# Kernel tuning notes

Hardware: AMD Instinct MI355X
Metric: run time of the kernel (lower is better)

## Reference

```python
import jax, jax.numpy as jnp
import numpy as np

B, S, D, H = 2, 2048, 1024, 16
HD = D // H

def setup_inputs() -> dict:
    key = jax.random.key(0)
    ks = jax.random.split(key, 9)
    s = 1.0 / np.sqrt(D)
    inp = {"x": jax.random.normal(ks[0], (B, S, D), dtype=jnp.float32)}
    for i, name in enumerate(["q", "k", "v", "o"]):
        inp[f"W_{name}"] = jax.random.uniform(ks[1 + 2 * i], (D, D), dtype=jnp.float32, minval=-s, maxval=s)
        inp[f"b_{name}"] = jax.random.uniform(ks[2 + 2 * i], (D,), dtype=jnp.float32, minval=-s, maxval=s)
    return inp


def reference(x, W_q, b_q, W_k, b_k, W_v, b_v, W_o, b_o):
    # x: [B, S, D]
    def split_heads(t):
        return t.reshape(B, S, H, HD).transpose(0, 2, 1, 3)  # [B, H, S, HD]

    Q = split_heads(x @ W_q + b_q)
    K = split_heads(x @ W_k + b_k)
    V = split_heads(x @ W_v + b_v)

    scale = 1.0 / np.sqrt(HD).astype(np.float32)
    scores = jnp.einsum("bhqd,bhkd->bhqk", Q, K) * scale  # [B, H, S, S]
    weights = jax.nn.softmax(scores, axis=-1)
    attn = jnp.einsum("bhqk,bhkd->bhqd", weights, V)  # [B, H, S, HD]
    attn = attn.transpose(0, 2, 1, 3).reshape(B, S, D)
    return attn @ W_o + b_o
```

## Files before the change

### kernel.cpp

```cpp
#include <hip/hip_runtime.h>
#include <hip/hip_bf16.h>

#define BB 2
#define SS 2048
#define DD 1024
#define HH 16
#define HD 64

typedef __attribute__((ext_vector_type(8))) short bf16x8;
typedef __attribute__((ext_vector_type(4))) float f32x4;

__device__ __forceinline__ unsigned short f2bf(float f) {
  unsigned int u = __float_as_uint(f);
  return (unsigned short)((u + 0x7FFFu + ((u >> 16) & 1u)) >> 16);
}

__device__ __forceinline__ float fast_exp2(float x) {
#if __has_builtin(__builtin_amdgcn_exp2f)
  return __builtin_amdgcn_exp2f(x);
#else
  return __expf(x * 0.6931471805599453f);
#endif
}

__device__ __forceinline__ void async_copy16(const unsigned short* gp, unsigned short* lp) {
  __builtin_amdgcn_global_load_lds(
      (const __attribute__((address_space(1))) unsigned int*)gp,
      (__attribute__((address_space(3))) unsigned int*)lp, 16, 0, 0);
}

__device__ __forceinline__ void pl32_swap(unsigned& a, unsigned& b) {
#if __has_builtin(__builtin_amdgcn_permlane32_swap)
  auto r = __builtin_amdgcn_permlane32_swap(a, b, false, false);
  a = r[0];
  b = r[1];
#else
  asm volatile("v_permlane32_swap_b32 %0, %1" : "+v"(a), "+v"(b));
#endif
}
__device__ __forceinline__ void pl16_swap(unsigned& a, unsigned& b) {
#if __has_builtin(__builtin_amdgcn_permlane16_swap)
  auto r = __builtin_amdgcn_permlane16_swap(a, b, false, false);
  a = r[0];
  b = r[1];
#else
  asm volatile("v_permlane16_swap_b32 %0, %1" : "+v"(a), "+v"(b));
#endif
}

__global__ __launch_bounds__(256) void prep_kernel(
    const float* __restrict__ x, unsigned short* __restrict__ xb,
    const float* __restrict__ W0, unsigned short* __restrict__ T0,
    const float* __restrict__ W1, unsigned short* __restrict__ T1,
    const float* __restrict__ W2, unsigned short* __restrict__ T2,
    const float* __restrict__ W3, unsigned short* __restrict__ T3) {
  const int blk = blockIdx.x;
  const int t = threadIdx.x;
  if (blk < 4096) {
    int i = blk * 1024 + t * 4;
    float4 v = *(const float4*)(x + i);
    ushort4 u;
    u.x = f2bf(v.x); u.y = f2bf(v.y); u.z = f2bf(v.z); u.w = f2bf(v.w);
    *(ushort4*)(xb + i) = u;
    return;
  }
  const int j = blk - 4096;
  const int jw = j >> 10;
  const int tb = j & 1023;
  const float* W = jw == 0 ? W0 : (jw == 1 ? W1 : (jw == 2 ? W2 : W3));
  unsigned short* T = jw == 0 ? T0 : (jw == 1 ? T1 : (jw == 2 ? T2 : T3));
  __shared__ float tile[32][33];
  int k0 = (tb & 31) * 32, n0 = (tb >> 5) * 32;
  int c = t & 31, r0 = t >> 5;
#pragma unroll
  for (int i = 0; i < 4; ++i) {
    int r = r0 + i * 8;
    tile[r][c] = W[(size_t)(k0 + r) * DD + n0 + c];
  }
  __syncthreads();
#pragma unroll
  for (int i = 0; i < 4; ++i) {
    int r = r0 + i * 8;
    T[(size_t)(n0 + r) * DD + k0 + c] = f2bf(tile[c][r]);
  }
}

template <int STORE>
__device__ __forceinline__ void gemm_core(
    const unsigned short* __restrict__ A, const unsigned short* __restrict__ BT,
    const float* __restrict__ bias, void* __restrict__ outp, float scale,
    int bm, int bn) {
  const int t = threadIdx.x;
  const int w = t >> 6;
  const int l = t & 63;
  const int wm = (w >> 1) * 64;
  const int wn = (w & 1) * 64;

  __shared__ __align__(16) unsigned short As[128 * 32];
  __shared__ __align__(16) unsigned short Bs[128 * 32];

  f32x4 acc[4][4];
#pragma unroll
  for (int i = 0; i < 4; ++i)
#pragma unroll
    for (int j = 0; j < 4; ++j) acc[i][j] = (f32x4)0.f;

  const int fr = l & 15;
  const int kg = (l >> 4) * 8;

  for (int k0 = 0; k0 < DD; k0 += 32) {
    __syncthreads();
#pragma unroll
    for (int c = 0; c < 2; ++c) {
      int e = (w * 2 + c) * 512 + l * 8;
      int row = e >> 5, kk = e & 31;
      async_copy16(A + (size_t)(bm + row) * DD + k0 + kk, As + (w * 2 + c) * 512);
      async_copy16(BT + (size_t)(bn + row) * DD + k0 + kk, Bs + (w * 2 + c) * 512);
    }
    __syncthreads();

    bf16x8 af[4], bfr[4];
#pragma unroll
    for (int i = 0; i < 4; ++i)
      af[i] = *(const bf16x8*)(As + (wm + i * 16 + fr) * 32 + kg);
#pragma unroll
    for (int j = 0; j < 4; ++j)
      bfr[j] = *(const bf16x8*)(Bs + (wn + j * 16 + fr) * 32 + kg);
#pragma unroll
    for (int i = 0; i < 4; ++i)
#pragma unroll
      for (int j = 0; j < 4; ++j)
        acc[i][j] = __builtin_amdgcn_mfma_f32_16x16x32_bf16(af[i], bfr[j], acc[i][j], 0, 0, 0);
  }

  const int col_l = l & 15;
  const int row_l = (l >> 4) * 4;

#pragma unroll
  for (int i = 0; i < 4; ++i) {
    int m_base = bm + wm + i * 16 + row_l;
#pragma unroll
    for (int j = 0; j < 4; ++j) {
      int n = bn + wn + j * 16 + col_l;
      float bv = bias[n];
      float* out = (float*)outp;
#pragma unroll
      for (int r = 0; r < 4; ++r)
        out[(size_t)(m_base + r) * DD + n] = acc[i][j][r] + bv;
    }
  }
}

__global__ __launch_bounds__(256) void out_gemm_mfma(
    const unsigned short* __restrict__ A, const unsigned short* __restrict__ WoT,
    const float* __restrict__ bo, float* __restrict__ out) {
  const int i = blockIdx.x;
  const int xcd = i & 7;
  const int slot = i >> 3;
  const int bm = (xcd + 8 * (slot >> 3)) * 128;
  const int bn = (slot & 7) * 128;
  gemm_core<0>(A, WoT, bo, (void*)out, 1.0f, bm, bn);
}

#define QPHASE(DB, KH, MH, S, VM) do {                                        \
    bf16x8 af[4];                                                             \
    _Pragma("unroll")                                                         \
    for (int ii = 0; ii < 4; ++ii) {                                          \
      int row = wm * 128 + (MH) * 64 + ii * 16 + fr;                          \
      int kb = kg16 ^ ((row & 8) ? 32 : 0) ^ ((row & 4) ? 16 : 0);            \
      af[ii] = *(const bf16x8*)((const char*)&lds[0][DB][KH][0] + row * 64 + kb); \
    }                                                                         \
    if ((MH) == 0) {                                                          \
      _Pragma("unroll")                                                       \
      for (int j = 0; j < 4; ++j) {                                           \
        int row = wn * 64 + j * 16 + fr;                                      \
        int kb = kg16 ^ ((row & 8) ? 32 : 0) ^ ((row & 4) ? 16 : 0);          \
        bfr[j] = *(const bf16x8*)((const char*)&lds[1][DB][KH][0] + row * 64 + kb); \
      }                                                                       \
    }                                                                         \
    stage_half(S);                                                            \
    asm volatile("s_barrier" ::: "memory");                                   \
    __builtin_amdgcn_s_setprio(1);                                            \
    _Pragma("unroll")                                                         \
    for (int ii = 0; ii < 4; ++ii)                                            \
      _Pragma("unroll")                                                       \
      for (int j = 0; j < 4; ++j)                                             \
        acc[(MH) * 4 + ii][j] = __builtin_amdgcn_mfma_f32_16x16x32_bf16(      \
            af[ii], bfr[j], acc[(MH) * 4 + ii][j], 0, 0, 0);                  \
    __builtin_amdgcn_s_setprio(0);                                            \
    if ((VM) == 1) asm volatile("s_waitcnt vmcnt(4)" ::: "memory");           \
    if ((VM) == 2) asm volatile("s_waitcnt vmcnt(0)" ::: "memory");           \
    asm volatile("s_barrier" ::: "memory");                                   \
  } while (0)

__global__ __launch_bounds__(512, 2) void qkv_gemm_8ph(
    const unsigned short* __restrict__ A,
    const unsigned short* __restrict__ WqT, const unsigned short* __restrict__ WkT,
    const unsigned short* __restrict__ WvT,
    const float* __restrict__ bq, const float* __restrict__ bk,
    const float* __restrict__ bv,
    unsigned short* __restrict__ Qo, unsigned short* __restrict__ Ko,
    unsigned short* __restrict__ VTo) {
  const int i = blockIdx.x;
  const int xcd = i & 7;
  const int slot = i >> 3;
  const int bmi = xcd * 2 + (slot / 12);
  const int c = slot % 12;
  const int which = c >> 2;
  const int bm = bmi * 256;
  const int bn = (c & 3) * 256;
  const unsigned short* BT = which == 0 ? WqT : (which == 1 ? WkT : WvT);
  const float* bias = which == 0 ? bq : (which == 1 ? bk : bv);

  const int t = threadIdx.x;
  const int w = t >> 6;
  const int l = t & 63;
  const int wm = w >> 2;
  const int wn = w & 3;
  const int fr = l & 15;
  const int kg16 = (l >> 4) * 16;

  __shared__ __align__(16) unsigned short lds[2][2][2][8192];

  f32x4 acc[8][4];
#pragma unroll
  for (int mi = 0; mi < 8; ++mi)
#pragma unroll
    for (int j = 0; j < 4; ++j) acc[mi][j] = (f32x4)0.f;

  auto stage_half = [&](int s) {
    if (s >= 64) return;
    const int Ts = s >> 2;
    const int db = Ts & 1;
    const int typ = s & 3;
    const int kh = typ >> 1;
    const int isB = typ & 1;
    const unsigned short* src = isB ? BT : A;
    const int rbase = isB ? bn : bm;
    unsigned short* dstbase = &lds[isB][db][kh][0];
    const int k0 = Ts * 64 + kh * 32;
#pragma unroll
    for (int j = 0; j < 2; ++j) {
      int cc = (w * 2 + j) * 64 + l;
      int row = cc >> 2;
      int ke = ((cc & 3) * 8) ^ ((row & 8) ? 16 : 0) ^ ((row & 4) ? 8 : 0);
      async_copy16(src + (size_t)(rbase + row) * DD + k0 + ke,
                   dstbase + (w * 2 + j) * 512);
    }
  };

  bf16x8 bfr[4];

  for (int s = 0; s < 6; ++s) stage_half(s);
  asm volatile("s_waitcnt vmcnt(4)" ::: "memory");
  asm volatile("s_barrier" ::: "memory");

  for (int T = 0; T < 14; ++T) {
    const int db = T & 1;
    const int sb = 4 * T + 6;
    QPHASE(db, 0, 0, sb + 0, 0);
    QPHASE(db, 0, 1, sb + 1, 0);
    QPHASE(db, 1, 0, sb + 2, 0);
    QPHASE(db, 1, 1, sb + 3, 1);
  }
  QPHASE(0, 0, 0, 62, 0);
  QPHASE(0, 0, 1, 63, 0);
  QPHASE(0, 1, 0, 64, 0);
  QPHASE(0, 1, 1, 64, 2);
  QPHASE(1, 0, 0, 64, 0);
  QPHASE(1, 0, 1, 64, 0);
  QPHASE(1, 1, 0, 64, 0);
  QPHASE(1, 1, 1, 64, 0);

  const int col_l = l & 15;
  const int row_l = (l >> 4) * 4;
  const int b_ = bm >> 11;

  if (which != 2) {
    const float scl = which == 0 ? 0.18033688011112042f : 1.0f;
    unsigned short* out = which == 0 ? Qo : Ko;
#pragma unroll
    for (int mi = 0; mi < 8; ++mi) {
      int m_base = bm + wm * 128 + mi * 16 + row_l;
#pragma unroll
      for (int j = 0; j < 4; ++j) {
        int n = bn + wn * 64 + j * 16 + col_l;
        float bv = bias[n];
        int h_ = n >> 6, hd_ = n & 63;
#pragma unroll
        for (int r = 0; r < 4; ++r) {
          int m = m_base + r;
          int b2 = m >> 11, s_ = m & 2047;
          out[(((size_t)(b2 * HH + h_) * SS) + s_) * HD + hd_] =
              f2bf((acc[mi][j][r] + bv) * scl);
        }
      }
    }
  } else {
    unsigned int* Tt = (unsigned int*)&lds[0][0][0][0];
#pragma unroll
    for (int mi = 0; mi < 8; ++mi) {
      int m2a = wm * 64 + mi * 8 + (l >> 4) * 2;
#pragma unroll
      for (int j = 0; j < 4; ++j) {
        int n = wn * 64 + j * 16 + col_l;
        float bv = bias[bn + n];
        uint2 dd;
        dd.x = (unsigned)f2bf(acc[mi][j][0] + bv) |
               ((unsigned)f2bf(acc[mi][j][1] + bv) << 16);
        dd.y = (unsigned)f2bf(acc[mi][j][2] + bv) |
               ((unsigned)f2bf(acc[mi][j][3] + bv) << 16);
        *(uint2*)(Tt + n * 128 + (m2a ^ ((n & 7) << 2))) = dd;
      }
    }
    __syncthreads();
    const int srow0 = bm & 2047;
    const int n_r = t >> 1;
    const int half = t & 1;
    const int n_glob = bn + n_r;
    const int h_ = n_glob >> 6, hd_ = n_glob & 63;
    unsigned short* ob =
        VTo + ((size_t)((b_ * HH + h_) * HD + hd_)) * SS + srow0 + half * 128;
#pragma unroll
    for (int cp = 0; cp < 16; ++cp) {
      uint4 v = *(const uint4*)(Tt + n_r * 128 +
                                ((half * 64 + cp * 4) ^ ((n_r & 7) << 2)));
      *(uint4*)(ob + cp * 8) = v;
    }
  }
}

__global__ __launch_bounds__(512, 4) void flash_attn_mfma(
    const unsigned short* __restrict__ Q,
    const unsigned short* __restrict__ K,
    const unsigned short* __restrict__ VT,
    unsigned short* __restrict__ ctx) {
  const int bh = blockIdx.x;
  const int qt = blockIdx.y;
  const int b  = bh >> 4;
  const int h  = bh & 15;
  const int t  = threadIdx.x;
  const int w  = t >> 6;
  const int l  = t & 63;
  const int wg = w & 3;
  const int wh = w >> 2;
  const int g  = l >> 4;
  const int ln = l & 15;

  const unsigned short* Qp = Q + ((size_t)bh * SS + (size_t)qt * 64 + wg * 16) * HD;
  const unsigned short* Kp = K + (size_t)bh * SS * HD;
  const unsigned short* Vp = VT + (size_t)bh * HD * SS;

  __shared__ __align__(16) unsigned short smem[2][2][2][2048];
  __shared__ __align__(16) float rred[4 * 64];

  bf16x8 qf[2];
#pragma unroll
  for (int kb = 0; kb < 2; ++kb)
    qf[kb] = *(const bf16x8*)(Qp + ln * HD + kb * 32 + g * 8);

  f32x4 o[4];
#pragma unroll
  for (int mt = 0; mt < 4; ++mt) o[mt] = (f32x4)0.f;
  float rs = 0.f;

  const int sp  = w >> 2;
  const int sq  = w & 3;
  const int idx = sq * 64 + l;
  const int rowK = idx >> 3;
  const int gccK = (idx & 7) ^ (rowK & 7);
  const unsigned short* kgp = Kp + (size_t)(sp * 32 + rowK) * HD + gccK * 8;
  const int rowV = idx >> 2;
  const int gc2V = (idx & 3) ^ ((rowV >> 1) & 3);
  const unsigned short* vgp = Vp + (size_t)rowV * SS + sp * 32 + gc2V * 8;
  unsigned short* dK = &smem[0][sp][0][sq * 512];
  unsigned short* dV = &smem[1][sp][0][sq * 512];

  int ko[2][2];
#pragma unroll
  for (int kb = 0; kb < 2; ++kb)
#pragma unroll
    for (int mt = 0; mt < 2; ++mt) {
      int row = mt * 16 + ln;
      ko[kb][mt] = row * 128 + (((kb * 4 + g) ^ (row & 7)) * 16);
    }
  int vo[4];
#pragma unroll
  for (int mt = 0; mt < 4; ++mt) {
    int row = mt * 16 + ln;
    vo[mt] = row * 64 + ((g ^ ((row >> 1) & 3)) * 16);
  }
  const char* kpar = (const char*)&smem[0][wh][0][0];
  const char* vpar = (const char*)&smem[1][wh][0][0];

  auto stage_i = [&](int db) {
    async_copy16(kgp, dK + db * 2048);
    async_copy16(vgp, dV + db * 2048);
    kgp += 64 * HD;
    vgp += 64;
  };

  auto body = [&](int db) {
    const char* Kst = kpar + db * 4096;
    const char* Vst = vpar + db * 4096;

    f32x4 st[2];
#pragma unroll
    for (int mt = 0; mt < 2; ++mt) st[mt] = (f32x4)0.f;
#pragma unroll
    for (int kb = 0; kb < 2; ++kb)
#pragma unroll
      for (int mt = 0; mt < 2; ++mt) {
        bf16x8 ka = *(const bf16x8*)(Kst + ko[kb][mt]);
        st[mt] = __builtin_amdgcn_mfma_f32_16x16x32_bf16(ka, qf[kb], st[mt], 0, 0, 0);
      }

    unsigned Sd[2][2];
#pragma unroll
    for (int mt = 0; mt < 2; ++mt) {
      float p0 = fast_exp2(st[mt][0]);
      float p1 = fast_exp2(st[mt][1]);
      float p2 = fast_exp2(st[mt][2]);
      float p3 = fast_exp2(st[mt][3]);
      Sd[mt][0] = __builtin_amdgcn_perm(__float_as_uint(p1), __float_as_uint(p0),
                                        0x07060302u);
      Sd[mt][1] = __builtin_amdgcn_perm(__float_as_uint(p3), __float_as_uint(p2),
                                        0x07060302u);
      rs += (p0 + p1) + (p2 + p3);
    }
#pragma unroll
    for (int p = 0; p < 2; ++p) pl32_swap(Sd[0][p], Sd[1][p]);
#pragma unroll
    for (int p = 0; p < 2; ++p) pl16_swap(Sd[0][p], Sd[1][p]);

    bf16x8 pbv;
    {
      union { unsigned u[4]; bf16x8 v; } cu;
      cu.u[0] = Sd[0][0];
      cu.u[1] = Sd[0][1];
      cu.u[2] = Sd[1][0];
      cu.u[3] = Sd[1][1];
      pbv = cu.v;
    }
#pragma unroll
    for (int mt = 0; mt < 4; ++mt) {
      bf16x8 va = *(const bf16x8*)(Vst + vo[mt]);
      o[mt] = __builtin_amdgcn_mfma_f32_16x16x32_bf16(va, pbv, o[mt], 0, 0, 0);
    }
  };

  stage_i(0);
  for (int kt2 = 0; kt2 < 16; ++kt2) {
    __syncthreads();
    stage_i(1);
    body(0);
    __syncthreads();
    if (kt2 < 15) stage_i(0);
    body(1);
  }

  __syncthreads();
  {
    float* ored = (float*)&smem[0][0][0][0];
    float* rb = ored + (wg * 64 + l) * 16;
    float* sb = rred + wg * 64 + l;
    if (wh == 1) {
#pragma unroll
      for (int mt = 0; mt < 4; ++mt)
        *(f32x4*)(rb + ((unsigned)(mt ^ (l & 3)) * 4)) = o[mt];
      sb[0] = rs;
    }
    __syncthreads();
    if (wh == 1) return;
#pragma unroll
    for (int mt = 0; mt < 4; ++mt) {
      f32x4 pv = *(const f32x4*)(rb + ((unsigned)(mt ^ (l & 3)) * 4));
      o[mt] += pv;
    }
    rs += sb[0];
  }

  {
    float lsum = rs;
    lsum += __shfl_xor(lsum, 16, 64);
    lsum += __shfl_xor(lsum, 32, 64);
    float inv = 1.f / lsum;
    int srow = qt * 64 + wg * 16 + ln;
    unsigned short* cb = ctx + (size_t)(b * SS + srow) * DD + h * HD;
#pragma unroll
    for (int mt = 0; mt < 4; ++mt) {
      ushort4 u4;
      u4.x = f2bf(o[mt][0] * inv);
      u4.y = f2bf(o[mt][1] * inv);
      u4.z = f2bf(o[mt][2] * inv);
      u4.w = f2bf(o[mt][3] * inv);
      *(ushort4*)(cb + mt * 16 + 4 * g) = u4;
    }
  }
}

extern "C" void kernel_launch(void* const* d_in, const int* in_sizes, int n_in,
                              void* d_out, int out_size, void* d_ws, size_t ws_size,
                              hipStream_t stream) {
  const float* x  = (const float*)d_in[0];
  const float* Wq = (const float*)d_in[1];
  const float* bq = (const float*)d_in[2];
  const float* Wk = (const float*)d_in[3];
  const float* bk = (const float*)d_in[4];
  const float* Wv = (const float*)d_in[5];
  const float* bv = (const float*)d_in[6];
  const float* Wo = (const float*)d_in[7];
  const float* bo = (const float*)d_in[8];
  float* out = (float*)d_out;

  const size_t ELEMS = (size_t)BB * SS * DD;
  char* ws = (char*)d_ws;
  unsigned short* xb   = (unsigned short*)ws;  ws += ELEMS * 2;
  unsigned short* WqT  = (unsigned short*)ws;  ws += (size_t)DD * DD * 2;
  unsigned short* WkT  = (unsigned short*)ws;  ws += (size_t)DD * DD * 2;
  unsigned short* WvT  = (unsigned short*)ws;  ws += (size_t)DD * DD * 2;
  unsigned short* WoT  = (unsigned short*)ws;  ws += (size_t)DD * DD * 2;
  unsigned short* Qb   = (unsigned short*)ws;  ws += ELEMS * 2;
  unsigned short* Kb   = (unsigned short*)ws;  ws += ELEMS * 2;
  unsigned short* VbT  = (unsigned short*)ws;  ws += ELEMS * 2;
  unsigned short* ctxb = (unsigned short*)ws;  ws += ELEMS * 2;

  prep_kernel<<<8192, 256, 0, stream>>>(x, xb, Wq, WqT, Wk, WkT, Wv, WvT, Wo, WoT);

  qkv_gemm_8ph<<<192, 512, 0, stream>>>(xb, WqT, WkT, WvT, bq, bk, bv,
                                        Qb, Kb, VbT);

  dim3 attn_grid(BB * HH, SS / 64);
  flash_attn_mfma<<<attn_grid, 512, 0, stream>>>(Qb, Kb, VbT, ctxb);

  out_gemm_mfma<<<256, 256, 0, stream>>>(ctxb, WoT, bo, out);
}
```

Baseline: 196.6 us.

## Rewrite QKV GEMM with 128x128 tiles and triple-buffered K pipeline

```diff
diff --git a/kernel.cpp b/kernel.cpp
--- a/kernel.cpp
+++ b/kernel.cpp
@@ -162,38 +162,7 @@
   gemm_core<0>(A, WoT, bo, (void*)out, 1.0f, bm, bn);
 }
 
-#define QPHASE(DB, KH, MH, S, VM) do {                                        \
-    bf16x8 af[4];                                                             \
-    _Pragma("unroll")                                                         \
-    for (int ii = 0; ii < 4; ++ii) {                                          \
-      int row = wm * 128 + (MH) * 64 + ii * 16 + fr;                          \
-      int kb = kg16 ^ ((row & 8) ? 32 : 0) ^ ((row & 4) ? 16 : 0);            \
-      af[ii] = *(const bf16x8*)((const char*)&lds[0][DB][KH][0] + row * 64 + kb); \
-    }                                                                         \
-    if ((MH) == 0) {                                                          \
-      _Pragma("unroll")                                                       \
-      for (int j = 0; j < 4; ++j) {                                           \
-        int row = wn * 64 + j * 16 + fr;                                      \
-        int kb = kg16 ^ ((row & 8) ? 32 : 0) ^ ((row & 4) ? 16 : 0);          \
-        bfr[j] = *(const bf16x8*)((const char*)&lds[1][DB][KH][0] + row * 64 + kb); \
-      }                                                                       \
-    }                                                                         \
-    stage_half(S);                                                            \
-    asm volatile("s_barrier" ::: "memory");                                   \
-    __builtin_amdgcn_s_setprio(1);                                            \
-    _Pragma("unroll")                                                         \
-    for (int ii = 0; ii < 4; ++ii)                                            \
-      _Pragma("unroll")                                                       \
-      for (int j = 0; j < 4; ++j)                                             \
-        acc[(MH) * 4 + ii][j] = __builtin_amdgcn_mfma_f32_16x16x32_bf16(      \
-            af[ii], bfr[j], acc[(MH) * 4 + ii][j], 0, 0, 0);                  \
-    __builtin_amdgcn_s_setprio(0);                                            \
-    if ((VM) == 1) asm volatile("s_waitcnt vmcnt(4)" ::: "memory");           \
-    if ((VM) == 2) asm volatile("s_waitcnt vmcnt(0)" ::: "memory");           \
-    asm volatile("s_barrier" ::: "memory");                                   \
-  } while (0)
-
-__global__ __launch_bounds__(512, 2) void qkv_gemm_8ph(
+__global__ __launch_bounds__(256, 3) void qkv_gemm_tri(
     const unsigned short* __restrict__ A,
     const unsigned short* __restrict__ WqT, const unsigned short* __restrict__ WkT,
     const unsigned short* __restrict__ WvT,
@@ -204,73 +173,86 @@
   const int i = blockIdx.x;
   const int xcd = i & 7;
   const int slot = i >> 3;
-  const int bmi = xcd * 2 + (slot / 12);
-  const int c = slot % 12;
-  const int which = c >> 2;
-  const int bm = bmi * 256;
-  const int bn = (c & 3) * 256;
+  const int bm = (xcd + 8 * (slot / 24)) * 128;
+  const int c = slot % 24;
+  const int which = c >> 3;
+  const int bn = (c & 7) * 128;
   const unsigned short* BT = which == 0 ? WqT : (which == 1 ? WkT : WvT);
   const float* bias = which == 0 ? bq : (which == 1 ? bk : bv);
 
   const int t = threadIdx.x;
   const int w = t >> 6;
   const int l = t & 63;
-  const int wm = w >> 2;
-  const int wn = w & 3;
+  const int wm = (w >> 1) * 64;
+  const int wn = (w & 1) * 64;
   const int fr = l & 15;
-  const int kg16 = (l >> 4) * 16;
-
-  __shared__ __align__(16) unsigned short lds[2][2][2][8192];
-
-  f32x4 acc[8][4];
-#pragma unroll
-  for (int mi = 0; mi < 8; ++mi)
-#pragma unroll
-    for (int j = 0; j < 4; ++j) acc[mi][j] = (f32x4)0.f;
-
-  auto stage_half = [&](int s) {
-    if (s >= 64) return;
-    const int Ts = s >> 2;
-    const int db = Ts & 1;
-    const int typ = s & 3;
-    const int kh = typ >> 1;
-    const int isB = typ & 1;
-    const unsigned short* src = isB ? BT : A;
-    const int rbase = isB ? bn : bm;
-    unsigned short* dstbase = &lds[isB][db][kh][0];
-    const int k0 = Ts * 64 + kh * 32;
-#pragma unroll
-    for (int j = 0; j < 2; ++j) {
-      int cc = (w * 2 + j) * 64 + l;
-      int row = cc >> 2;
-      int ke = ((cc & 3) * 8) ^ ((row & 8) ? 16 : 0) ^ ((row & 4) ? 8 : 0);
-      async_copy16(src + (size_t)(rbase + row) * DD + k0 + ke,
-                   dstbase + (w * 2 + j) * 512);
-    }
+  const int kgB = (l >> 4) * 16;
+
+  __shared__ __align__(16) unsigned short lds[2][3][4096];
+
+  f32x4 acc[4][4];
+#pragma unroll
+  for (int ii = 0; ii < 4; ++ii)
+#pragma unroll
+    for (int j = 0; j < 4; ++j) acc[ii][j] = (f32x4)0.f;
+
+  int aoff[4], boff[4];
+#pragma unroll
+  for (int ii = 0; ii < 4; ++ii) {
+    aoff[ii] = (wm + ii * 16 + fr) * 64 + kgB;
+    boff[ii] = (wn + ii * 16 + fr) * 64 + kgB;
+  }
+
+  const int cc0 = w * 128 + l;
+  const int cc1 = cc0 + 64;
+  const int row0 = cc0 >> 2, kk0 = (cc0 & 3) * 8;
+  const int row1 = cc1 >> 2, kk1 = (cc1 & 3) * 8;
+  const unsigned short* a0 = A + (size_t)(bm + row0) * DD + kk0;
+  const unsigned short* a1 = A + (size_t)(bm + row1) * DD + kk1;
+  const unsigned short* b0 = BT + (size_t)(bn + row0) * DD + kk0;
+  const unsigned short* b1 = BT + (size_t)(bn + row1) * DD + kk1;
+
+  auto stage_tile = [&](int T) {
+    if (T >= 32) return;
+    const int buf = T % 3;
+    const int k0 = T * 32;
+    async_copy16(a0 + k0, &lds[0][buf][w * 1024]);
+    async_copy16(a1 + k0, &lds[0][buf][w * 1024 + 512]);
+    async_copy16(b0 + k0, &lds[1][buf][w * 1024]);
+    async_copy16(b1 + k0, &lds[1][buf][w * 1024 + 512]);
   };
 
-  bf16x8 bfr[4];
-
-  for (int s = 0; s < 6; ++s) stage_half(s);
+  auto phase = [&](int T, int vm) {
+    const int buf = T % 3;
+    const char* Ab = (const char*)&lds[0][buf][0];
+    const char* Bb = (const char*)&lds[1][buf][0];
+    bf16x8 af[4], bfr[4];
+#pragma unroll
+    for (int ii = 0; ii < 4; ++ii) af[ii] = *(const bf16x8*)(Ab + aoff[ii]);
+#pragma unroll
+    for (int j = 0; j < 4; ++j) bfr[j] = *(const bf16x8*)(Bb + boff[j]);
+    stage_tile(T + 2);
+    asm volatile("s_barrier" ::: "memory");
+    __builtin_amdgcn_s_setprio(1);
+#pragma unroll
+    for (int ii = 0; ii < 4; ++ii)
+#pragma unroll
+      for (int j = 0; j < 4; ++j)
+        acc[ii][j] = __builtin_amdgcn_mfma_f32_16x16x32_bf16(af[ii], bfr[j], acc[ii][j], 0, 0, 0);
+    __builtin_amdgcn_s_setprio(0);
+    if (vm == 1) asm volatile("s_waitcnt vmcnt(4)" ::: "memory");
+    if (vm == 2) asm volatile("s_waitcnt vmcnt(0)" ::: "memory");
+    asm volatile("s_barrier" ::: "memory");
+  };
+
+  stage_tile(0);
+  stage_tile(1);
   asm volatile("s_waitcnt vmcnt(4)" ::: "memory");
   asm volatile("s_barrier" ::: "memory");
 
-  for (int T = 0; T < 14; ++T) {
-    const int db = T & 1;
-    const int sb = 4 * T + 6;
-    QPHASE(db, 0, 0, sb + 0, 0);
-    QPHASE(db, 0, 1, sb + 1, 0);
-    QPHASE(db, 1, 0, sb + 2, 0);
-    QPHASE(db, 1, 1, sb + 3, 1);
-  }
-  QPHASE(0, 0, 0, 62, 0);
-  QPHASE(0, 0, 1, 63, 0);
-  QPHASE(0, 1, 0, 64, 0);
-  QPHASE(0, 1, 1, 64, 2);
-  QPHASE(1, 0, 0, 64, 0);
-  QPHASE(1, 0, 1, 64, 0);
-  QPHASE(1, 1, 0, 64, 0);
-  QPHASE(1, 1, 1, 64, 0);
+  for (int T = 0; T < 30; ++T) phase(T, 1);
+  phase(30, 2);
+  phase(31, 0);
 
   const int col_l = l & 15;
   const int row_l = (l >> 4) * 4;
@@ -280,11 +262,11 @@
     const float scl = which == 0 ? 0.18033688011112042f : 1.0f;
     unsigned short* out = which == 0 ? Qo : Ko;
 #pragma unroll
-    for (int mi = 0; mi < 8; ++mi) {
-      int m_base = bm + wm * 128 + mi * 16 + row_l;
+    for (int ii = 0; ii < 4; ++ii) {
+      int m_base = bm + wm + ii * 16 + row_l;
 #pragma unroll
       for (int j = 0; j < 4; ++j) {
-        int n = bn + wn * 64 + j * 16 + col_l;
+        int n = bn + wn + j * 16 + col_l;
         float bv = bias[n];
         int h_ = n >> 6, hd_ = n & 63;
 #pragma unroll
@@ -292,40 +274,48 @@
           int m = m_base + r;
           int b2 = m >> 11, s_ = m & 2047;
           out[(((size_t)(b2 * HH + h_) * SS) + s_) * HD + hd_] =
-              f2bf((acc[mi][j][r] + bv) * scl);
+              f2bf((acc[ii][j][r] + bv) * scl);
         }
       }
     }
   } else {
-    unsigned int* Tt = (unsigned int*)&lds[0][0][0][0];
-#pragma unroll
-    for (int mi = 0; mi < 8; ++mi) {
-      int m2a = wm * 64 + mi * 8 + (l >> 4) * 2;
-#pragma unroll
-      for (int j = 0; j < 4; ++j) {
-        int n = wn * 64 + j * 16 + col_l;
-        float bv = bias[bn + n];
-        uint2 dd;
-        dd.x = (unsigned)f2bf(acc[mi][j][0] + bv) |
-               ((unsigned)f2bf(acc[mi][j][1] + bv) << 16);
-        dd.y = (unsigned)f2bf(acc[mi][j][2] + bv) |
-               ((unsigned)f2bf(acc[mi][j][3] + bv) << 16);
-        *(uint2*)(Tt + n * 128 + (m2a ^ ((n & 7) << 2))) = dd;
+    unsigned short* out = VTo;
+    unsigned int* Tt = (unsigned int*)&lds[0][0][0];
+    const int srow0 = bm & 2047;
+#pragma unroll
+    for (int p = 0; p < 4; ++p) {
+      __syncthreads();
+      if ((w & 1) == (p >> 1)) {
+        const int jt0 = (p & 1) * 2;
+#pragma unroll
+        for (int jj = 0; jj < 2; ++jj) {
+          int jt = jt0 + jj;
+          int n_p = jj * 16 + col_l;
+          float bv = bias[bn + p * 32 + n_p];
+#pragma unroll
+          for (int ii = 0; ii < 4; ++ii) {
+            int m0 = wm + ii * 16 + row_l;
+#pragma unroll
+            for (int pr = 0; pr < 2; ++pr) {
+              unsigned int val =
+                  (unsigned int)f2bf(acc[ii][jt][2 * pr] + bv) |
+                  ((unsigned int)f2bf(acc[ii][jt][2 * pr + 1] + bv) << 16);
+              int m = m0 + 2 * pr;
+              Tt[n_p * 64 + (((m >> 1)) ^ ((n_p & 7) << 2))] = val;
+            }
+          }
+        }
       }
-    }
-    __syncthreads();
-    const int srow0 = bm & 2047;
-    const int n_r = t >> 1;
-    const int half = t & 1;
-    const int n_glob = bn + n_r;
-    const int h_ = n_glob >> 6, hd_ = n_glob & 63;
-    unsigned short* ob =
-        VTo + ((size_t)((b_ * HH + h_) * HD + hd_)) * SS + srow0 + half * 128;
-#pragma unroll
-    for (int cp = 0; cp < 16; ++cp) {
-      uint4 v = *(const uint4*)(Tt + n_r * 128 +
-                                ((half * 64 + cp * 4) ^ ((n_r & 7) << 2)));
-      *(uint4*)(ob + cp * 8) = v;
+      __syncthreads();
+#pragma unroll
+      for (int cq = 0; cq < 2; ++cq) {
+        int q = t + cq * 256;
+        int n_p = q >> 4, cpos = q & 15;
+        uint4 v = *(const uint4*)(Tt + n_p * 64 + ((cpos * 4) ^ ((n_p & 7) << 2)));
+        int n_glob = bn + p * 32 + n_p;
+        int h_ = n_glob >> 6, hd_ = n_glob & 63;
+        *(uint4*)(out + ((size_t)((b_ * HH + h_) * HD + hd_)) * SS + srow0 + cpos * 8) = v;
+      }
     }
   }
 }
@@ -527,7 +517,7 @@
 
   prep_kernel<<<8192, 256, 0, stream>>>(x, xb, Wq, WqT, Wk, WkT, Wv, WvT, Wo, WoT);
 
-  qkv_gemm_8ph<<<192, 512, 0, stream>>>(xb, WqT, WkT, WvT, bq, bk, bv,
+  qkv_gemm_tri<<<768, 256, 0, stream>>>(xb, WqT, WkT, WvT, bq, bk, bv,
                                         Qb, Kb, VbT);
 
   dim3 attn_grid(BB * HH, SS / 64);
```

Result: no change. 193.7 us (-1.5%).
